# Kernel tuning notes

Measured on AMD Instinct MI355X. Metric: run time of the kernel, lower is better.

## Reference

```python
import jax, jax.numpy as jnp
import numpy as np

# ---- dims mirroring MovingNCA(num_classes=10, num_hidden=16, size_image=(512,512), size_neo=(510,510)) ----
N = 512; M = 512                 # full image/state grid
N_NEO = 510; M_NEO = 510         # active cell grid (= N-2, M-2)
N_ACTIVE = N - 2                 # perceptions clipped to [0, N_ACTIVE-1]
IMG_CH = 1; ACT_CH = 2
NUM_HIDDEN = 16; NUM_CLASSES = 10
INPUT_DIM = IMG_CH + NUM_HIDDEN + NUM_CLASSES      # 27 channels per patch pixel
OUTPUT_DIM = NUM_HIDDEN + NUM_CLASSES + ACT_CH     # 28
STATE_CH = INPUT_DIM - IMG_CH                      # 26
FEAT = 9 * INPUT_DIM + 2                           # 245 = 3*3*input_dim + 2 pos features
ITERS = 4
THRESH = 0.0007                                    # custom_round_slicing threshold


def setup_inputs() -> dict:
    key = jax.random.key(0)
    k1, k2, k3 = jax.random.split(key, 3)
    img = jax.random.uniform(k1, (N, M, IMG_CH), jnp.float32)
    state0 = jnp.zeros((N, M, STATE_CH), jnp.float32)
    # get_perception_matrix with size_neo = size_image - 2 -> identity grid over active area
    gx, gy = jnp.meshgrid(jnp.arange(N_NEO), jnp.arange(M_NEO), indexing='ij')
    perceptions0 = jnp.stack([gx, gy], axis=-1).astype(jnp.int32)
    W1 = jax.random.normal(k2, (FEAT, FEAT), jnp.float32) / np.sqrt(FEAT)
    b1 = jnp.zeros((FEAT,), jnp.float32)
    W2 = jax.random.normal(k3, (FEAT, OUTPUT_DIM), jnp.float32) / np.sqrt(FEAT)
    b2 = jnp.zeros((OUTPUT_DIM,), jnp.float32)
    return {"img": img, "state0": state0, "perceptions0": perceptions0,
            "W1": W1, "b1": b1, "W2": W2, "b2": b2}


def _nca_step(img, W1, b1, W2, b2, state, perc):
    d = jnp.arange(3)
    # gather 3x3 image patches at (moving) perception positions: [Nn, Mn, 3, 3, 1]
    xi = perc[..., 0][:, :, None, None] + d[None, None, :, None]
    yi = perc[..., 1][:, :, None, None] + d[None, None, None, :]
    perc_img = img[xi, yi, :]
    # gather 3x3 state (comms) patches at fixed grid positions: [Nn, Mn, 3, 3, C]
    sx = (jnp.arange(N_NEO)[:, None] + d[None, :])[:, None, :, None]   # [Nn,1,3,1]
    sy = (jnp.arange(M_NEO)[:, None] + d[None, :])[None, :, None, :]   # [1,Mn,1,3]
    comms = state[sx, sy, :]
    # flatten order matches np.concatenate((perc, comms), axis=2).flatten()
    feat = jnp.concatenate([perc_img, comms], axis=-1).reshape(N_NEO * M_NEO, 9 * INPUT_DIM)
    # CURRENT_POS=True branch of collect_input
    posx = ((perc[..., 0] - N // 2) / (N // 2)).astype(feat.dtype).reshape(-1, 1)
    posy = ((perc[..., 1] - M // 2) / (M // 2)).astype(feat.dtype).reshape(-1, 1)
    inp = jnp.concatenate([feat, posx, posy], axis=1)                  # [Nn*Mn, 245]
    guesses = (inp @ W1 + b1) @ W2 + b2                                # two linear Dense layers
    outputs = guesses.reshape(N_NEO, M_NEO, OUTPUT_DIM)
    # scatter-add state update on interior
    state = state.at[1:1 + N_NEO, 1:1 + M_NEO, :].add(outputs[..., :STATE_CH])
    # moving: custom sign-rounding of action then clip to active grid
    action = outputs[..., -ACT_CH:]
    delta = jnp.where(action < -THRESH, -1, jnp.where(action > THRESH, 1, 0)).astype(perc.dtype)
    perc = jnp.clip(perc + delta, 0, N_ACTIVE - 1)
    return state, perc, guesses


def reference(img, state0, perceptions0, W1, b1, W2, b2):
    def body(carry, _):
        state, perc, _ = carry
        state, perc, guesses = _nca_step(img, W1, b1, W2, b2, state, perc)
        return (state, perc, guesses), None
    g0 = jnp.zeros((N_NEO * M_NEO, OUTPUT_DIM), jnp.float32)
    (state, perc, guesses), _ = jax.lax.scan(jax.checkpoint(body),
                                             (state0, perceptions0, g0), None, length=ITERS)
    # classify() returns (class channels of interior state, last guesses)
    return state[1:1 + N_NEO, 1:1 + M_NEO, -NUM_CLASSES:], guesses
```

## Files before the change

### kernel.cpp

```cpp
#include <hip/hip_runtime.h>

#define NN 512
#define MM 512
#define NEO 510
#define PLANE (NN * MM)
#define STATE_CH 26
#define OUT_DIM 28
#define FEAT 245
#define NW (FEAT * OUT_DIM)
#define THRESH 0.0007f

__global__ __launch_bounds__(256) void prep_all(
    const float* __restrict__ s0, float* __restrict__ A, float* __restrict__ B,
    const float* __restrict__ W1, const float* __restrict__ b1,
    const float* __restrict__ W2, const float* __restrict__ b2,
    float* __restrict__ W12, float* __restrict__ b12) {
  if (blockIdx.x < 256) {
    const int base = (blockIdx.x * 256 + threadIdx.x) * 4;
    float v[4][STATE_CH];
    const float* src = s0 + (size_t)base * STATE_CH;
#pragma unroll
    for (int q = 0; q < 4; ++q)
#pragma unroll
      for (int c = 0; c < STATE_CH; ++c) v[q][c] = src[q * STATE_CH + c];
#pragma unroll
    for (int c = 0; c < STATE_CH; ++c) {
      float4 w = make_float4(v[0][c], v[1][c], v[2][c], v[3][c]);
      *(float4*)(A + (size_t)c * PLANE + base) = w;
      *(float4*)(B + (size_t)c * PLANE + base) = w;
    }
  } else {
    const int t = (blockIdx.x - 256) * 256 + threadIdx.x;
    if (t < NW) {
      const int f = t / OUT_DIM, k = t - f * OUT_DIM;
      float s = 0.0f;
      for (int jj = 0; jj < FEAT; ++jj) s = fmaf(W1[f * FEAT + jj], W2[jj * OUT_DIM + k], s);
      W12[t] = s;
    } else if (t < NW + OUT_DIM) {
      const int k = t - NW;
      float s = b2[k];
      for (int jj = 0; jj < FEAT; ++jj) s = fmaf(b1[jj], W2[jj * OUT_DIM + k], s);
      b12[k] = s;
    }
  }
}

#define LOADV(V, RP, IP)                                             \
  {                                                                  \
    V[0] = *(IP);                                                    \
    _Pragma("unroll") for (int c = 0; c < STATE_CH; ++c)             \
        V[1 + c] = (RP)[c * PLANE];                                  \
  }

#define FMABLK(V, WP)                                                \
  {                                                                  \
    _Pragma("unroll") for (int t = 0; t < 27; ++t) {                 \
      const float vt = V[t];                                         \
      _Pragma("unroll") for (int k = 0; k < OUT_DIM; ++k)            \
          acc[k] = fmaf(vt, (WP)[t * OUT_DIM + k], acc[k]);          \
    }                                                                \
  }

#define ADVANCE()                                                    \
  {                                                                  \
    const int d = (djc == 2) ? (MM - 2) : 1;                         \
    djc = (djc == 2) ? 0 : djc + 1;                                  \
    rp += d; ip += d;                                                \
  }

template <bool LAST>
__global__ __launch_bounds__(256, 4) void nca_step(
    const float* __restrict__ img, const float* __restrict__ sold, float* __restrict__ snew,
    const int* __restrict__ pold, int* __restrict__ pnew,
    const float* __restrict__ W12, const float* __restrict__ b12,
    float* __restrict__ out0, float* __restrict__ out1) {
  const int bid = (int)blockIdx.x;
  const int lin = (bid & 7) * 128 + (bid >> 3);
  const int ib = lin >> 3;
  const int jb = lin & 7;
  const int lane = (int)(threadIdx.x & 63);
  const int wv   = (int)(threadIdx.x >> 6);
  const int i = ib * 4 + wv;
  const int j = jb * 64 + lane;
  if (i >= NEO || j >= NEO) return;
  const int cell = i * NEO + j;
  const int2 p = ((const int2*)pold)[cell];

  float acc[OUT_DIM];
#pragma unroll
  for (int k = 0; k < OUT_DIM; ++k) acc[k] = b12[k];

  const float* rp = sold + i * MM + j;
  const float* ip = img + p.x * MM + p.y;
  const float* wp = W12;
  int djc = 0;
  float va[27], vb[27];

  LOADV(va, rp, ip);
#pragma unroll 1
  for (int pr = 0; pr < 4; ++pr) {
    ADVANCE();
    LOADV(vb, rp, ip);
    FMABLK(va, wp); wp += 27 * OUT_DIM;
    ADVANCE();
    LOADV(va, rp, ip);
    FMABLK(vb, wp); wp += 27 * OUT_DIM;
  }
  FMABLK(va, wp); wp += 27 * OUT_DIM;

  const float posx = (float)(p.x - 256) * (1.0f / 256.0f);
  const float posy = (float)(p.y - 256) * (1.0f / 256.0f);
#pragma unroll
  for (int k = 0; k < OUT_DIM; ++k) acc[k] = fmaf(posx, wp[k], acc[k]);
#pragma unroll
  for (int k = 0; k < OUT_DIM; ++k) acc[k] = fmaf(posy, wp[OUT_DIM + k], acc[k]);

  const int nb = (i + 1) * MM + (j + 1);
  if (!LAST) {
    const float ax = acc[26], ay = acc[27];
    int dx = (ax < -THRESH) ? -1 : ((ax > THRESH) ? 1 : 0);
    int dy = (ay < -THRESH) ? -1 : ((ay > THRESH) ? 1 : 0);
    int nx = min(max(p.x + dx, 0), NEO - 1);
    int ny = min(max(p.y + dy, 0), NEO - 1);
    ((int2*)pnew)[cell] = make_int2(nx, ny);
#pragma unroll
    for (int c = 0; c < STATE_CH; ++c)
      snew[c * PLANE + nb] = sold[c * PLANE + nb] + acc[c];
  } else {
    float2* o0 = (float2*)(out0 + (size_t)cell * 10);
#pragma unroll
    for (int c = 0; c < 5; ++c) {
      float2 v;
      v.x = sold[(16 + 2 * c) * PLANE + nb] + acc[16 + 2 * c];
      v.y = sold[(17 + 2 * c) * PLANE + nb] + acc[17 + 2 * c];
      o0[c] = v;
    }
    float4* o1 = (float4*)(out1 + (size_t)cell * OUT_DIM);
#pragma unroll
    for (int q = 0; q < 7; ++q)
      o1[q] = make_float4(acc[4 * q], acc[4 * q + 1], acc[4 * q + 2], acc[4 * q + 3]);
  }
}

extern "C" void kernel_launch(void* const* d_in, const int* in_sizes, int n_in,
                              void* d_out, int out_size, void* d_ws, size_t ws_size,
                              hipStream_t stream) {
  const float* img    = (const float*)d_in[0];
  const float* state0 = (const float*)d_in[1];
  const int*   perc0  = (const int*)d_in[2];
  const float* W1     = (const float*)d_in[3];
  const float* b1     = (const float*)d_in[4];
  const float* W2     = (const float*)d_in[5];
  const float* b2     = (const float*)d_in[6];
  float* out = (float*)d_out;

  float* stateA = (float*)d_ws;
  float* stateB = stateA + (size_t)STATE_CH * PLANE;
  int*   percA  = (int*)(stateB + (size_t)STATE_CH * PLANE);
  int*   percB  = percA + (size_t)NEO * NEO * 2;
  float* W12    = (float*)(percB + (size_t)NEO * NEO * 2);
  float* b12    = W12 + NW;

  float* out0 = out;
  float* out1 = out + (size_t)NEO * NEO * 10;

  prep_all<<<dim3(256 + 27), dim3(256), 0, stream>>>(state0, stateA, stateB,
                                                     W1, b1, W2, b2, W12, b12);

  dim3 grid(1024), block(256);
  nca_step<false><<<grid, block, 0, stream>>>(img, stateA, stateB, perc0, percB, W12, b12, nullptr, nullptr);
  nca_step<false><<<grid, block, 0, stream>>>(img, stateB, stateA, percB, percA, W12, b12, nullptr, nullptr);
  nca_step<false><<<grid, block, 0, stream>>>(img, stateA, stateB, percA, percB, W12, b12, nullptr, nullptr);
  nca_step<true ><<<grid, block, 0, stream>>>(img, stateB, nullptr, percB, nullptr, W12, b12, out0, out1);
}
```

Baseline: 324.3 us.

## Compute four rows per thread to reuse each weight load across cells

```diff
diff --git a/kernel.cpp b/kernel.cpp
--- a/kernel.cpp
+++ b/kernel.cpp
@@ -45,100 +45,122 @@
   }
 }
 
-#define LOADV(V, RP, IP)                                             \
-  {                                                                  \
-    V[0] = *(IP);                                                    \
-    _Pragma("unroll") for (int c = 0; c < STATE_CH; ++c)             \
-        V[1 + c] = (RP)[c * PLANE];                                  \
+#define POSEPI(ACC, Q)                                                        \
+  {                                                                           \
+    const float px = (float)(pq[Q].x - 256) * (1.0f / 256.0f);                \
+    const float py = (float)(pq[Q].y - 256) * (1.0f / 256.0f);                \
+    _Pragma("unroll") for (int k = 0; k < OUT_DIM; ++k)                       \
+        ACC[k] = fmaf(px, wp[k], ACC[k]);                                     \
+    _Pragma("unroll") for (int k = 0; k < OUT_DIM; ++k)                       \
+        ACC[k] = fmaf(py, wp[OUT_DIM + k], ACC[k]);                           \
   }
 
-#define FMABLK(V, WP)                                                \
-  {                                                                  \
-    _Pragma("unroll") for (int t = 0; t < 27; ++t) {                 \
-      const float vt = V[t];                                         \
-      _Pragma("unroll") for (int k = 0; k < OUT_DIM; ++k)            \
-          acc[k] = fmaf(vt, (WP)[t * OUT_DIM + k], acc[k]);          \
-    }                                                                \
+#define STORE_STEP(ACC, Q)                                                    \
+  if (act[Q]) {                                                               \
+    const int nb = nbs[Q];                                                    \
+    const float ax = ACC[26], ay = ACC[27];                                   \
+    int dx = (ax < -THRESH) ? -1 : ((ax > THRESH) ? 1 : 0);                   \
+    int dy = (ay < -THRESH) ? -1 : ((ay > THRESH) ? 1 : 0);                   \
+    int nx = min(max(pq[Q].x + dx, 0), NEO - 1);                              \
+    int ny = min(max(pq[Q].y + dy, 0), NEO - 1);                              \
+    ((int2*)pnew)[cells[Q]] = make_int2(nx, ny);                              \
+    _Pragma("unroll") for (int c = 0; c < STATE_CH; ++c)                      \
+        snew[c * PLANE + nb] = sold[c * PLANE + nb] + ACC[c];                 \
   }
 
-#define ADVANCE()                                                    \
-  {                                                                  \
-    const int d = (djc == 2) ? (MM - 2) : 1;                         \
-    djc = (djc == 2) ? 0 : djc + 1;                                  \
-    rp += d; ip += d;                                                \
+#define STORE_LAST(ACC, Q)                                                    \
+  if (act[Q]) {                                                               \
+    const int nb = nbs[Q];                                                    \
+    float2* o0 = (float2*)(out0 + (size_t)cells[Q] * 10);                     \
+    _Pragma("unroll") for (int c = 0; c < 5; ++c) {                           \
+      float2 v;                                                               \
+      v.x = sold[(16 + 2 * c) * PLANE + nb] + ACC[16 + 2 * c];                \
+      v.y = sold[(17 + 2 * c) * PLANE + nb] + ACC[17 + 2 * c];                \
+      o0[c] = v;                                                              \
+    }                                                                         \
+    float4* o1 = (float4*)(out1 + (size_t)cells[Q] * OUT_DIM);                \
+    _Pragma("unroll") for (int r = 0; r < 7; ++r)                             \
+        o1[r] = make_float4(ACC[4 * r], ACC[4 * r + 1], ACC[4 * r + 2],       \
+                            ACC[4 * r + 3]);                                  \
   }
 
 template <bool LAST>
-__global__ __launch_bounds__(256, 4) void nca_step(
+__global__ __launch_bounds__(256, 2) void nca_step(
     const float* __restrict__ img, const float* __restrict__ sold, float* __restrict__ snew,
     const int* __restrict__ pold, int* __restrict__ pnew,
     const float* __restrict__ W12, const float* __restrict__ b12,
     float* __restrict__ out0, float* __restrict__ out1) {
   const int bid = (int)blockIdx.x;
-  const int lin = (bid & 7) * 128 + (bid >> 3);
-  const int ib = lin >> 3;
-  const int jb = lin & 7;
+  const int lin = (bid & 7) * 32 + (bid >> 3);
+  const int band = lin >> 3;
+  const int jb   = lin & 7;
   const int lane = (int)(threadIdx.x & 63);
   const int wv   = (int)(threadIdx.x >> 6);
-  const int i = ib * 4 + wv;
   const int j = jb * 64 + lane;
-  if (i >= NEO || j >= NEO) return;
-  const int cell = i * NEO + j;
-  const int2 p = ((const int2*)pold)[cell];
+  if (j >= NEO) return;
 
-  float acc[OUT_DIM];
+  int2 pq[4]; const float* rp[4]; const float* ip[4];
+  bool act[4]; int cells[4]; int nbs[4];
 #pragma unroll
-  for (int k = 0; k < OUT_DIM; ++k) acc[k] = b12[k];
+  for (int q = 0; q < 4; ++q) {
+    const int iq = band * 16 + wv + 4 * q;
+    act[q] = (iq < NEO);
+    const int ic = act[q] ? iq : (NEO - 1);
+    cells[q] = ic * NEO + j;
+    nbs[q] = (ic + 1) * MM + (j + 1);
+    pq[q] = ((const int2*)pold)[cells[q]];
+    rp[q] = sold + ic * MM + j;
+    ip[q] = img + pq[q].x * MM + pq[q].y;
+  }
 
-  const float* rp = sold + i * MM + j;
-  const float* ip = img + p.x * MM + p.y;
+  float acc0[OUT_DIM], acc1[OUT_DIM], acc2[OUT_DIM], acc3[OUT_DIM];
+#pragma unroll
+  for (int k = 0; k < OUT_DIM; ++k) {
+    const float b = b12[k];
+    acc0[k] = b; acc1[k] = b; acc2[k] = b; acc3[k] = b;
+  }
+
   const float* wp = W12;
   int djc = 0;
-  float va[27], vb[27];
+  float sl[3][4];
 
-  LOADV(va, rp, ip);
 #pragma unroll 1
-  for (int pr = 0; pr < 4; ++pr) {
-    ADVANCE();
-    LOADV(vb, rp, ip);
-    FMABLK(va, wp); wp += 27 * OUT_DIM;
-    ADVANCE();
-    LOADV(va, rp, ip);
-    FMABLK(vb, wp); wp += 27 * OUT_DIM;
+  for (int ps = 0; ps < 9; ++ps) {
+#pragma unroll
+    for (int q = 0; q < 4; ++q) sl[0][q] = *ip[q];
+#pragma unroll
+    for (int q = 0; q < 4; ++q) sl[1][q] = rp[q][0];
+#pragma unroll
+    for (int t = 0; t < 27; ++t) {
+      if (t < 25) {
+#pragma unroll
+        for (int q = 0; q < 4; ++q) sl[(t + 2) % 3][q] = rp[q][(t + 1) * PLANE];
+      }
+      const float* wt = wp + t * OUT_DIM;
+#pragma unroll
+      for (int k = 0; k < OUT_DIM; ++k) {
+        const float w = wt[k];
+        acc0[k] = fmaf(sl[t % 3][0], w, acc0[k]);
+        acc1[k] = fmaf(sl[t % 3][1], w, acc1[k]);
+        acc2[k] = fmaf(sl[t % 3][2], w, acc2[k]);
+        acc3[k] = fmaf(sl[t % 3][3], w, acc3[k]);
+      }
+    }
+    wp += 27 * OUT_DIM;
+    if (ps != 8) {
+      const int d = (djc == 2) ? (MM - 2) : 1;
+      djc = (djc == 2) ? 0 : djc + 1;
+#pragma unroll
+      for (int q = 0; q < 4; ++q) { rp[q] += d; ip[q] += d; }
+    }
   }
-  FMABLK(va, wp); wp += 27 * OUT_DIM;
 
-  const float posx = (float)(p.x - 256) * (1.0f / 256.0f);
-  const float posy = (float)(p.y - 256) * (1.0f / 256.0f);
-#pragma unroll
-  for (int k = 0; k < OUT_DIM; ++k) acc[k] = fmaf(posx, wp[k], acc[k]);
-#pragma unroll
-  for (int k = 0; k < OUT_DIM; ++k) acc[k] = fmaf(posy, wp[OUT_DIM + k], acc[k]);
+  POSEPI(acc0, 0) POSEPI(acc1, 1) POSEPI(acc2, 2) POSEPI(acc3, 3)
 
-  const int nb = (i + 1) * MM + (j + 1);
   if (!LAST) {
-    const float ax = acc[26], ay = acc[27];
-    int dx = (ax < -THRESH) ? -1 : ((ax > THRESH) ? 1 : 0);
-    int dy = (ay < -THRESH) ? -1 : ((ay > THRESH) ? 1 : 0);
-    int nx = min(max(p.x + dx, 0), NEO - 1);
-    int ny = min(max(p.y + dy, 0), NEO - 1);
-    ((int2*)pnew)[cell] = make_int2(nx, ny);
-#pragma unroll
-    for (int c = 0; c < STATE_CH; ++c)
-      snew[c * PLANE + nb] = sold[c * PLANE + nb] + acc[c];
+    STORE_STEP(acc0, 0) STORE_STEP(acc1, 1) STORE_STEP(acc2, 2) STORE_STEP(acc3, 3)
   } else {
-    float2* o0 = (float2*)(out0 + (size_t)cell * 10);
-#pragma unroll
-    for (int c = 0; c < 5; ++c) {
-      float2 v;
-      v.x = sold[(16 + 2 * c) * PLANE + nb] + acc[16 + 2 * c];
-      v.y = sold[(17 + 2 * c) * PLANE + nb] + acc[17 + 2 * c];
-      o0[c] = v;
-    }
-    float4* o1 = (float4*)(out1 + (size_t)cell * OUT_DIM);
-#pragma unroll
-    for (int q = 0; q < 7; ++q)
-      o1[q] = make_float4(acc[4 * q], acc[4 * q + 1], acc[4 * q + 2], acc[4 * q + 3]);
+    STORE_LAST(acc0, 0) STORE_LAST(acc1, 1) STORE_LAST(acc2, 2) STORE_LAST(acc3, 3)
   }
 }
 
@@ -167,7 +189,7 @@
   prep_all<<<dim3(256 + 27), dim3(256), 0, stream>>>(state0, stateA, stateB,
                                                      W1, b1, W2, b2, W12, b12);
 
-  dim3 grid(1024), block(256);
+  dim3 grid(256), block(256);
   nca_step<false><<<grid, block, 0, stream>>>(img, stateA, stateB, perc0, percB, W12, b12, nullptr, nullptr);
   nca_step<false><<<grid, block, 0, stream>>>(img, stateB, stateA, percB, percA, W12, b12, nullptr, nullptr);
   nca_step<false><<<grid, block, 0, stream>>>(img, stateA, stateB, percA, percB, W12, b12, nullptr, nullptr);
```

Measured after the change: 1.104 ms. 3.4x slower.
